# Kernel optimization log

Hardware: AMD Instinct MI355X
Metric: run time of the kernel (lower is better)

The kernel has to match this reference:

```python
import jax, jax.numpy as jnp
import numpy as np

# ---- module constants (from init_kwargs) ----
NATOMS = 600
NBINS = 64
CUTOFF = 7.5            # raw cutoff passed to __init__
CELL_L = 20.0           # cubic box edge (diagonal cell)
PI = float(np.pi)

BINS = jnp.linspace(0.0, CUTOFF, NBINS + 1)                 # [nbins+1]
VOL_BINS = 4.0 * PI / 3.0 * (BINS[1:] ** 3 - BINS[:-1] ** 3)  # [nbins]
CUTOFF_ADJ = CUTOFF + float(BINS[1] - BINS[0]) * 2.0        # self.cutoff after init
CELL = jnp.array([CELL_L, CELL_L, CELL_L], dtype=jnp.float32)  # diag of cell

# GaussianSmearing(start=0, stop=cutoff, n_gaussians=nbins, trainable=False)
G_OFFSETS = jnp.linspace(0.0, CUTOFF, NBINS)                # [nbins]
G_WIDTH = float(G_OFFSETS[1] - G_OFFSETS[0])
G_COEFF = -0.5 / (G_WIDTH ** 2)


def setup_inputs() -> dict:
    key = jax.random.key(0)
    # positions uniformly inside the cubic box [0, L)^3
    xyz = jax.random.uniform(key, (4, NATOMS, 3), dtype=jnp.float32) * CELL_L
    return {"xyz": xyz}


def reference(xyz):
    # pairwise differences: [B, N, N, 3]
    dis_mat = xyz[:, None, :, :] - xyz[:, :, None, :]
    # minimum-image PBC wrap
    offsets = (-(dis_mat >= 0.5 * CELL).astype(xyz.dtype)
               + (dis_mat < -0.5 * CELL).astype(xyz.dtype))
    dis_mat = dis_mat + offsets * CELL
    dis_sq = jnp.sum(dis_mat * dis_mat, axis=-1)            # [B, N, N]
    mask = (dis_sq < CUTOFF_ADJ ** 2) & (dis_sq != 0.0)     # [B, N, N]
    # safe sqrt (masked-out entries contribute zero below)
    pair_dis = jnp.sqrt(jnp.where(mask, dis_sq, 1.0))       # [B, N, N]
    # Gaussian smear -> soft histogram: sum over all valid pairs
    gauss = jnp.exp(G_COEFF * (pair_dis[..., None] - G_OFFSETS) ** 2)  # [B,N,N,nbins]
    count = jnp.sum(mask[..., None].astype(xyz.dtype) * gauss, axis=(0, 1, 2))  # [nbins]
    count = count / jnp.sum(count)
    rdf_val = count / (2.0 * VOL_BINS / (2.0 * CUTOFF_ADJ) ** 3)
    return (BINS, rdf_val)
```

## Files before the change

kernel.cpp:

```cpp
#include <hip/hip_runtime.h>
#include <math.h>

#define NATOMS 600
#define NBINS  64
#define NBATCH 4
#define NROWS  (NBATCH * NATOMS)
#define NREPL  32

constexpr float CELL_L     = 20.0f;
constexpr float INV_CELL   = 1.0f / 20.0f;
constexpr float BIN_W      = 7.5f / 64.0f;
constexpr float CUTOFF_ADJ = 7.5f + 2.0f * BIN_W;
constexpr float CUT2       = CUTOFF_ADJ * CUTOFF_ADJ;
constexpr float G_SPACING  = 7.5f / 63.0f;
constexpr float G_COEFF    = -0.5f / (G_SPACING * G_SPACING);
constexpr float PI_F       = 3.14159265358979323846f;

__global__ __launch_bounds__(256) void rdf_pairs(const float* __restrict__ xyz,
                                                 float* __restrict__ repl) {
    __shared__ float sflat[NATOMS * 3];
    __shared__ float sred[256];

    const int tid  = threadIdx.x;
    const int wave = tid >> 6;
    const int lane = tid & 63;
    const int row  = blockIdx.x;
    const int b    = row / NATOMS;
    const int i    = row - b * NATOMS;

    const float* g = xyz + (size_t)b * NATOMS * 3;
    for (int t = tid; t < NATOMS * 3; t += 256) sflat[t] = g[t];
    __syncthreads();

    const float xi = sflat[3 * i + 0];
    const float yi = sflat[3 * i + 1];
    const float zi = sflat[3 * i + 2];
    const float off = (float)lane * G_SPACING;
    float acc = 0.0f;

    const int jbeg = wave * (NATOMS / 4);
    const int jend = jbeg + (NATOMS / 4);

    for (int j0 = jbeg; j0 < jend; j0 += 64) {
        const int j = j0 + lane;
        const bool valid = j < jend;
        const int jj = valid ? j : 0;
        float dx = sflat[3 * jj + 0] - xi;
        float dy = sflat[3 * jj + 1] - yi;
        float dz = sflat[3 * jj + 2] - zi;
        dx -= CELL_L * rintf(dx * INV_CELL);
        dy -= CELL_L * rintf(dy * INV_CELL);
        dz -= CELL_L * rintf(dz * INV_CELL);
        const float r2 = dx * dx + dy * dy + dz * dz;
        const float d  = sqrtf(r2);
        unsigned long long m = __ballot(valid && (r2 < CUT2) && (r2 != 0.0f));
        while (m) {
            const int k = (int)__builtin_ctzll(m);
            m &= m - 1;
            const float dk = __int_as_float(
                __builtin_amdgcn_readlane(__float_as_int(d), k));
            const float t = dk - off;
            acc += __expf(G_COEFF * t * t);
        }
    }

    sred[tid] = acc;
    __syncthreads();
    if (tid < NBINS) {
        const float s = sred[tid] + sred[64 + tid] + sred[128 + tid] +
                        sred[192 + tid];
        atomicAdd(&repl[(blockIdx.x & (NREPL - 1)) * NBINS + tid], s);
    }
}

__global__ __launch_bounds__(64) void rdf_finalize(const float* __restrict__ repl,
                                                   float* __restrict__ out) {
    const int lane = threadIdx.x;
    const float poison = __uint_as_float(0xAAAAAAAAu);
    float c = -(float)NREPL * poison;
    #pragma unroll
    for (int r = 0; r < NREPL; ++r) c += repl[r * NBINS + lane];

    float total = c;
    #pragma unroll
    for (int o = 32; o > 0; o >>= 1) total += __shfl_xor(total, o, 64);

    out[lane] = (float)lane * BIN_W;
    if (lane == 0) out[64] = 7.5f;

    const float b0 = (float)lane * BIN_W;
    const float b1 = (float)(lane + 1) * BIN_W;
    const float vol = (4.0f * PI_F / 3.0f) * (b1 * b1 * b1 - b0 * b0 * b0);
    const float diam = 2.0f * CUTOFF_ADJ;
    const float denom = 2.0f * vol / (diam * diam * diam);
    out[65 + lane] = (c / total) / denom;
}

extern "C" void kernel_launch(void* const* d_in, const int* in_sizes, int n_in,
                              void* d_out, int out_size, void* d_ws, size_t ws_size,
                              hipStream_t stream) {
    const float* xyz = (const float*)d_in[0];
    float* out = (float*)d_out;
    float* repl = (float*)d_ws;

    rdf_pairs<<<dim3(NROWS), dim3(256), 0, stream>>>(xyz, repl);
    rdf_finalize<<<dim3(1), dim3(64), 0, stream>>>(repl, out);
}
```

Before: 65.49 us.

## Assign one atom row per wave and compact hit distances through LDS

Each wave now owns a full row i and scans all 600 j atoms, instead of a block splitting one row across four waves. This cuts the grid from 2400 to 600 blocks, so the xyz staging into shared memory is amortized over four rows. In-cutoff distances are stream-compacted into a per-wave LDS buffer using ballot and mbcnt, which replaces the serial ctz/readlane loop with a plain unrolled loop over shared memory. Each wave then atomically adds its 64 bins directly, removing the block reduction and its barrier. In exchange there are more atomics per block and fewer blocks to keep the GPU occupied.

```diff
diff --git a/kernel.cpp b/kernel.cpp
--- a/kernel.cpp
+++ b/kernel.cpp
@@ -6,6 +6,7 @@
 #define NBATCH 4
 #define NROWS  (NBATCH * NATOMS)
 #define NREPL  32
+#define RPB    150
 
 constexpr float CELL_L     = 20.0f;
 constexpr float INV_CELL   = 1.0f / 20.0f;
@@ -19,31 +20,28 @@
 __global__ __launch_bounds__(256) void rdf_pairs(const float* __restrict__ xyz,
                                                  float* __restrict__ repl) {
     __shared__ float sflat[NATOMS * 3];
-    __shared__ float sred[256];
+    __shared__ float shits[4][NATOMS + 8];
 
     const int tid  = threadIdx.x;
     const int wave = tid >> 6;
     const int lane = tid & 63;
-    const int row  = blockIdx.x;
-    const int b    = row / NATOMS;
-    const int i    = row - b * NATOMS;
+    const int bid  = blockIdx.x;
+    const int b    = bid / RPB;
+    const int g    = bid - b * RPB;
+    const int i    = g * 4 + wave;
 
-    const float* g = xyz + (size_t)b * NATOMS * 3;
-    for (int t = tid; t < NATOMS * 3; t += 256) sflat[t] = g[t];
+    const float* gp = xyz + (size_t)b * NATOMS * 3;
+    for (int t = tid; t < NATOMS * 3; t += 256) sflat[t] = gp[t];
     __syncthreads();
 
     const float xi = sflat[3 * i + 0];
     const float yi = sflat[3 * i + 1];
     const float zi = sflat[3 * i + 2];
-    const float off = (float)lane * G_SPACING;
-    float acc = 0.0f;
 
-    const int jbeg = wave * (NATOMS / 4);
-    const int jend = jbeg + (NATOMS / 4);
-
-    for (int j0 = jbeg; j0 < jend; j0 += 64) {
+    int nh = 0;
+    for (int j0 = 0; j0 < NATOMS; j0 += 64) {
         const int j = j0 + lane;
-        const bool valid = j < jend;
+        const bool valid = j < NATOMS;
         const int jj = valid ? j : 0;
         float dx = sflat[3 * jj + 0] - xi;
         float dy = sflat[3 * jj + 1] - yi;
@@ -53,24 +51,24 @@
         dz -= CELL_L * rintf(dz * INV_CELL);
         const float r2 = dx * dx + dy * dy + dz * dz;
         const float d  = sqrtf(r2);
-        unsigned long long m = __ballot(valid && (r2 < CUT2) && (r2 != 0.0f));
-        while (m) {
-            const int k = (int)__builtin_ctzll(m);
-            m &= m - 1;
-            const float dk = __int_as_float(
-                __builtin_amdgcn_readlane(__float_as_int(d), k));
-            const float t = dk - off;
-            acc += __expf(G_COEFF * t * t);
-        }
+        const bool hit = valid && (r2 < CUT2) && (r2 != 0.0f);
+        const unsigned long long m = __ballot(hit);
+        const int prefix = __builtin_amdgcn_mbcnt_hi(
+            (unsigned)(m >> 32), __builtin_amdgcn_mbcnt_lo((unsigned)m, 0));
+        if (hit) shits[wave][nh + prefix] = d;
+        nh += (int)__popcll(m);
     }
 
-    sred[tid] = acc;
-    __syncthreads();
-    if (tid < NBINS) {
-        const float s = sred[tid] + sred[64 + tid] + sred[128 + tid] +
-                        sred[192 + tid];
-        atomicAdd(&repl[(blockIdx.x & (NREPL - 1)) * NBINS + tid], s);
+    const float off = (float)lane * G_SPACING;
+    float acc = 0.0f;
+    #pragma unroll 4
+    for (int h = 0; h < nh; ++h) {
+        const float t = shits[wave][h] - off;
+        acc += __expf(G_COEFF * t * t);
     }
+
+    const int gw = (bid << 2) | wave;
+    atomicAdd(&repl[(gw & (NREPL - 1)) * NBINS + lane], acc);
 }
 
 __global__ __launch_bounds__(64) void rdf_finalize(const float* __restrict__ repl,
@@ -103,6 +101,6 @@
     float* out = (float*)d_out;
     float* repl = (float*)d_ws;
 
-    rdf_pairs<<<dim3(NROWS), dim3(256), 0, stream>>>(xyz, repl);
+    rdf_pairs<<<dim3(NBATCH * RPB), dim3(256), 0, stream>>>(xyz, repl);
     rdf_finalize<<<dim3(1), dim3(64), 0, stream>>>(repl, out);
 }
```

Result: no change. 65.10 us (-0.6%).
